# Performance work log

Hardware: AMD Instinct MI355X
Metric: run time of the kernel (lower is better)

## Reference

```python
import jax, jax.numpy as jnp
import numpy as np

M_TOP = 30      # top-M candidates per query
K_NB = 20       # K+1 nearest within candidate set (K=19)
BETA = 0.15


def setup_inputs() -> dict:
    key = jax.random.key(0)
    k1, k2, k3 = jax.random.split(key, 3)
    N, D, B, R = 500000, 512, 4096, 1000
    X = jax.random.normal(k1, (N, D), dtype=jnp.float32)
    Q = jax.random.normal(k2, (B, D), dtype=jnp.float32)
    ranks = jax.random.randint(k3, (R, B), 0, N, dtype=jnp.int64)
    return {"X": X, "Q": Q, "ranks": ranks}


def reference(X, Q, ranks):
    # ranks: [n_ranked, B] -> take top-M candidate ids per query: [B, M]
    rt = ranks.T[:, :M_TOP]                       # [B, M]
    Xt = X[rt]                                    # gather: [B, M, D]
    # batched self-similarity among the M candidates
    sim = jnp.einsum('bmd,bnd->bmn', Xt, Xt)      # [B, M, M]
    # descending sort, keep top K_NB values+indices (== -sort(-sim)[:K], argsort(-sim)[:K])
    vals, idx = jax.lax.top_k(sim, K_NB)          # [B, M, K]
    # weights: first neighbor (self) weight 1.0, rest scaled by beta
    w = jnp.concatenate([jnp.ones_like(vals[..., :1]), vals[..., 1:] * BETA], axis=-1)
    w = w[..., None]                              # [B, M, K, 1]
    # gather neighbor descriptors within each query's candidate set
    # x_g[b,m,k,d] = Xt[b, idx[b,m,k], d]
    x_g = jnp.take_along_axis(Xt[:, None, :, :], idx[..., None], axis=2)  # [B, M, K, D]
    # weighted average over the K neighbors
    x_dba = jnp.sum(x_g * w, axis=2) / jnp.sum(w, axis=2)                 # [B, M, D]
    # rerank candidates against the query descriptor
    scores = jnp.einsum('bd,bmd->bm', Q, x_dba)   # [B, M]
    order = jnp.argsort(-scores, axis=-1)         # [B, M]
    rerank = jnp.take_along_axis(rt, order, axis=1)  # [B, M] final db ids
    return rerank, scores, order, x_dba
```

## Files before the change

### kernel.cpp

```cpp
#include <hip/hip_runtime.h>
#include <stdint.h>

#define MT   30
#define KNB  20
#define DD   512
#define SROW 68
#define WSTRIDE 960

#define PR(r) ((((r) & 1) * 15) + ((r) >> 1))

extern "C" __global__ void __launch_bounds__(256, 8)
mdesc_decide(const float* __restrict__ X, const float* __restrict__ Q,
             const int* __restrict__ ranks, float* __restrict__ out,
             float* __restrict__ wsF, int B)
{
    __shared__ alignas(16) char arrA[MT * SROW * 4];
    __shared__ alignas(16) float QS[DD];
    __shared__ double simS[MT][MT + 1];
    __shared__ double qdotPart[MT][8];
    __shared__ double qdotS[MT];
    __shared__ int    rtS[MT];

    float  (*XtS)[SROW] = (float(*)[SROW])arrA;
    float  (*MwS)[MT]   = (float(*)[MT])arrA;
    double *scoreS      = (double*)(arrA + 3600);
    int    *orderS      = (int*)(arrA + 3840);

    const int b = blockIdx.x;
    const int tid = threadIdx.x;

    if (tid < MT) rtS[tid] = ranks[(size_t)tid * B + b];
    __syncthreads();

    const bool isSim = (tid < 120);
    const bool isQ   = (tid >= 128 && tid < 248);
    int i0 = 0, i1 = 0, j0 = 0, j1 = 0;
    if (isSim) {
        int I = 0, rem = tid;
        while (rem >= 15 - I) { rem -= 15 - I; ++I; }
        int J = I + rem;
        i0 = 2 * I; i1 = i0 + 1; j0 = 2 * J; j1 = j0 + 1;
    }
    const int qm = (tid - 128) >> 2;
    const int qs = (tid - 128) & 3;

    double a00 = 0.0, a01 = 0.0, a10 = 0.0, a11 = 0.0;

    for (int st = 0; st < 8; ++st) {
        for (int i = tid; i < MT * 16; i += 256) {
            int row = i >> 4;
            int k = i & 15;
            float4 v = *(const float4*)(X + (size_t)rtS[row] * DD + st * 64 + (k << 2));
            *(float4*)(&XtS[PR(row)][k << 2]) = v;
        }
        if (st == 0 && tid < 128) {
            float4 v = *(const float4*)(Q + (size_t)b * DD + (tid << 2));
            *(float4*)(&QS[tid << 2]) = v;
        }
        __syncthreads();

        if (isSim) {
            const float* R0 = &XtS[PR(i0)][0];
            const float* R1 = &XtS[PR(i1)][0];
            const float* C0 = &XtS[PR(j0)][0];
            const float* C1 = &XtS[PR(j1)][0];
            for (int k = 0; k < 16; ++k) {
                float4 va0 = *(const float4*)(R0 + (k << 2));
                float4 va1 = *(const float4*)(R1 + (k << 2));
                float4 vb0 = *(const float4*)(C0 + (k << 2));
                float4 vb1 = *(const float4*)(C1 + (k << 2));
                const float* A0 = (const float*)&va0;
                const float* A1 = (const float*)&va1;
                const float* B0 = (const float*)&vb0;
                const float* B1 = (const float*)&vb1;
                #pragma unroll
                for (int c = 0; c < 4; ++c) {
                    double x0 = (double)A0[c], x1 = (double)A1[c];
                    double y0 = (double)B0[c], y1 = (double)B1[c];
                    a00 = fma(x0, y0, a00);
                    a01 = fma(x0, y1, a01);
                    a10 = fma(x1, y0, a10);
                    a11 = fma(x1, y1, a11);
                }
            }
            if (st == 3) {
                simS[i0][j0] = a00; simS[i0][j1] = a01;
                simS[i1][j0] = a10; simS[i1][j1] = a11;
                a00 = a01 = a10 = a11 = 0.0;
            }
            if (st == 7) {
                double s00 = simS[i0][j0] + a00;
                double s01 = simS[i0][j1] + a01;
                double s10 = simS[i1][j0] + a10;
                double s11 = simS[i1][j1] + a11;
                simS[i0][j0] = s00; simS[j0][i0] = s00;
                simS[i0][j1] = s01; simS[j1][i0] = s01;
                simS[i1][j0] = s10; simS[j0][i1] = s10;
                simS[i1][j1] = s11; simS[j1][i1] = s11;
            }
        }
        if (isQ && (st & 3) == qs) {
            double acc = 0.0;
            const float* xr = &XtS[PR(qm)][0];
            for (int k = 0; k < 16; ++k) {
                float4 q4 = *(const float4*)(&QS[(st * 16 + k) << 2]);
                float4 x4 = *(const float4*)(xr + (k << 2));
                const float* qq = (const float*)&q4;
                const float* xx = (const float*)&x4;
                #pragma unroll
                for (int c = 0; c < 4; ++c)
                    acc = fma((double)qq[c], (double)xx[c], acc);
            }
            qdotPart[qm][st] = acc;
        }
        __syncthreads();
    }

    for (int i = tid; i < MT * MT; i += 256) (&MwS[0][0])[i] = 0.0f;
    __syncthreads();

    const size_t sec = (size_t)B * MT;
    if (tid < MT) {
        {
            double acc = 0.0;
            #pragma unroll
            for (int s = 0; s < 8; ++s) acc += qdotPart[tid][s];
            qdotS[tid] = acc;
        }
        const int m = tid;
        unsigned used = 0;
        double Wsum = 0.0, sAcc = 0.0;
        for (int k = 0; k < KNB; ++k) {
            double best = -1.0e300; int bj = 0;
            for (int j = 0; j < MT; ++j) {
                if (used & (1u << j)) continue;
                double v = simS[m][j];
                if (v > best) { best = v; bj = j; }
            }
            used |= (1u << bj);
            double w = (k == 0) ? 1.0 : best * 0.15;
            Wsum += w;
            sAcc = fma(w, qdotS[bj], sAcc);
            MwS[m][bj] = (float)w;
        }
        scoreS[m] = sAcc / Wsum;
        float inv = (float)(1.0 / Wsum);
        for (int j = 0; j < MT; ++j)
            if (used & (1u << j)) MwS[m][j] *= inv;
        double mysc = scoreS[tid];
        int pos = 0;
        for (int j = 0; j < MT; ++j) {
            double v = scoreS[j];
            if (v > mysc || (v == mysc && j < tid)) ++pos;
        }
        orderS[pos] = tid;
        int r = tid;
        int src = orderS[r];
        out[(size_t)b * MT + r]            = (float)rtS[src];
        out[sec + (size_t)b * MT + tid]    = (float)scoreS[tid];
        out[2 * sec + (size_t)b * MT + r]  = (float)src;
    }
    __syncthreads();

    for (int i = tid; i < MT * MT; i += 256)
        wsF[(size_t)b * WSTRIDE + i] = (&MwS[0][0])[i];
}

extern "C" __global__ void __launch_bounds__(256)
mdesc_xdba(const float* __restrict__ X, const int* __restrict__ ranks,
           const float* __restrict__ wsF, float* __restrict__ out, int B)
{
    __shared__ float wS[MT][MT];
    __shared__ int   rtS[MT];

    const int b = blockIdx.x;
    const int tid = threadIdx.x;

    if (tid < MT) rtS[tid] = ranks[(size_t)tid * B + b];
    for (int i = tid; i < MT * MT; i += 256)
        (&wS[0][0])[i] = wsF[(size_t)b * WSTRIDE + i];
    __syncthreads();

    const int c  = tid & 127;
    const int g  = tid >> 7;
    const int r0 = g * 15;

    float4 acc[15];
    #pragma unroll
    for (int r = 0; r < 15; ++r) acc[r] = make_float4(0.f, 0.f, 0.f, 0.f);

    for (int j = 0; j < MT; ++j) {
        float4 xv = *(const float4*)(X + (size_t)rtS[j] * DD + (c << 2));
        #pragma unroll
        for (int r = 0; r < 15; ++r) {
            float wj = wS[r0 + r][j];
            acc[r].x = fmaf(wj, xv.x, acc[r].x);
            acc[r].y = fmaf(wj, xv.y, acc[r].y);
            acc[r].z = fmaf(wj, xv.z, acc[r].z);
            acc[r].w = fmaf(wj, xv.w, acc[r].w);
        }
    }

    const size_t xbase = 3 * (size_t)B * MT;
    #pragma unroll
    for (int r = 0; r < 15; ++r) {
        *(float4*)(out + xbase + ((size_t)b * MT + (r0 + r)) * DD + (c << 2)) = acc[r];
    }
}

extern "C" void kernel_launch(void* const* d_in, const int* in_sizes, int n_in,
                              void* d_out, int out_size, void* d_ws, size_t ws_size,
                              hipStream_t stream)
{
    const float* X = (const float*)d_in[0];
    const float* Q = (const float*)d_in[1];
    const int* ranks = (const int*)d_in[2];
    const int B = in_sizes[1] / DD;
    float* wsF = (float*)d_ws;
    mdesc_decide<<<dim3(B), dim3(256), 0, stream>>>(X, Q, ranks, (float*)d_out, wsF, B);
    mdesc_xdba<<<dim3(B), dim3(256), 0, stream>>>(X, ranks, wsF, (float*)d_out, B);
}
```

Measured before the change: 275.0 us.

## Fuse neighbor-selection and weighted-average kernels into one launch

Merges the decision kernel and the x_dba accumulation kernel into a single kernel, keeping the weight matrix in shared memory (padded to 32 columns) instead of writing it to a workspace and reloading it. This removes one kernel launch and a global round trip of the weights. The inner loop now processes two candidate rows per iteration with float2 weight loads. Launch bounds drop from 8 to 6 waves per SIMD, which allows more registers but may lower occupancy. Fusing also serialises the latency-bound gather phase behind the selection phase within each block.

Result: faster. 248.6 us, median of 2 (-9.6%).

```diff
diff --git a/kernel.cpp b/kernel.cpp
--- a/kernel.cpp
+++ b/kernel.cpp
@@ -5,14 +5,13 @@
 #define KNB  20
 #define DD   512
 #define SROW 68
-#define WSTRIDE 960
+#define MWS  32
 
 #define PR(r) ((((r) & 1) * 15) + ((r) >> 1))
 
-extern "C" __global__ void __launch_bounds__(256, 8)
-mdesc_decide(const float* __restrict__ X, const float* __restrict__ Q,
-             const int* __restrict__ ranks, float* __restrict__ out,
-             float* __restrict__ wsF, int B)
+extern "C" __global__ void __launch_bounds__(256, 6)
+mdesc_fused(const float* __restrict__ X, const float* __restrict__ Q,
+            const int* __restrict__ ranks, float* __restrict__ out, int B)
 {
     __shared__ alignas(16) char arrA[MT * SROW * 4];
     __shared__ alignas(16) float QS[DD];
@@ -22,9 +21,9 @@
     __shared__ int    rtS[MT];
 
     float  (*XtS)[SROW] = (float(*)[SROW])arrA;
-    float  (*MwS)[MT]   = (float(*)[MT])arrA;
-    double *scoreS      = (double*)(arrA + 3600);
-    int    *orderS      = (int*)(arrA + 3840);
+    float  (*MwS)[MWS]  = (float(*)[MWS])arrA;
+    double *scoreS      = (double*)(arrA + 3840);
+    int    *orderS      = (int*)(arrA + 4080);
 
     const int b = blockIdx.x;
     const int tid = threadIdx.x;
@@ -116,7 +115,7 @@
         __syncthreads();
     }
 
-    for (int i = tid; i < MT * MT; i += 256) (&MwS[0][0])[i] = 0.0f;
+    for (int i = tid; i < MT * MWS; i += 256) (&MwS[0][0])[i] = 0.0f;
     __syncthreads();
 
     const size_t sec = (size_t)B * MT;
@@ -162,49 +161,37 @@
     }
     __syncthreads();
 
-    for (int i = tid; i < MT * MT; i += 256)
-        wsF[(size_t)b * WSTRIDE + i] = (&MwS[0][0])[i];
-}
-
-extern "C" __global__ void __launch_bounds__(256)
-mdesc_xdba(const float* __restrict__ X, const int* __restrict__ ranks,
-           const float* __restrict__ wsF, float* __restrict__ out, int B)
-{
-    __shared__ float wS[MT][MT];
-    __shared__ int   rtS[MT];
-
-    const int b = blockIdx.x;
-    const int tid = threadIdx.x;
-
-    if (tid < MT) rtS[tid] = ranks[(size_t)tid * B + b];
-    for (int i = tid; i < MT * MT; i += 256)
-        (&wS[0][0])[i] = wsF[(size_t)b * WSTRIDE + i];
-    __syncthreads();
-
-    const int c  = tid & 127;
-    const int g  = tid >> 7;
-    const int r0 = g * 15;
-
-    float4 acc[15];
-    #pragma unroll
-    for (int r = 0; r < 15; ++r) acc[r] = make_float4(0.f, 0.f, 0.f, 0.f);
-
-    for (int j = 0; j < MT; ++j) {
-        float4 xv = *(const float4*)(X + (size_t)rtS[j] * DD + (c << 2));
+    {
+        const int sub = tid >> 7;
+        const int c   = tid & 127;
+        const int r0  = sub * 15;
+        float4 acc[15];
+        #pragma unroll
+        for (int r = 0; r < 15; ++r) acc[r] = make_float4(0.f, 0.f, 0.f, 0.f);
+
+        for (int jg = 0; jg < 15; ++jg) {
+            const int ja = 2 * jg, jb = ja + 1;
+            float4 xv0 = *(const float4*)(X + (size_t)rtS[ja] * DD + (c << 2));
+            float4 xv1 = *(const float4*)(X + (size_t)rtS[jb] * DD + (c << 2));
+            #pragma unroll
+            for (int r = 0; r < 15; ++r) {
+                float2 wv = *(const float2*)&MwS[r0 + r][ja];
+                acc[r].x = fmaf(wv.x, xv0.x, acc[r].x);
+                acc[r].x = fmaf(wv.y, xv1.x, acc[r].x);
+                acc[r].y = fmaf(wv.x, xv0.y, acc[r].y);
+                acc[r].y = fmaf(wv.y, xv1.y, acc[r].y);
+                acc[r].z = fmaf(wv.x, xv0.z, acc[r].z);
+                acc[r].z = fmaf(wv.y, xv1.z, acc[r].z);
+                acc[r].w = fmaf(wv.x, xv0.w, acc[r].w);
+                acc[r].w = fmaf(wv.y, xv1.w, acc[r].w);
+            }
+        }
+
+        const size_t xbase = 3 * sec;
         #pragma unroll
         for (int r = 0; r < 15; ++r) {
-            float wj = wS[r0 + r][j];
-            acc[r].x = fmaf(wj, xv.x, acc[r].x);
-            acc[r].y = fmaf(wj, xv.y, acc[r].y);
-            acc[r].z = fmaf(wj, xv.z, acc[r].z);
-            acc[r].w = fmaf(wj, xv.w, acc[r].w);
-        }
-    }
-
-    const size_t xbase = 3 * (size_t)B * MT;
-    #pragma unroll
-    for (int r = 0; r < 15; ++r) {
-        *(float4*)(out + xbase + ((size_t)b * MT + (r0 + r)) * DD + (c << 2)) = acc[r];
+            *(float4*)(out + xbase + ((size_t)b * MT + (r0 + r)) * DD + (c << 2)) = acc[r];
+        }
     }
 }
 
@@ -216,7 +203,5 @@
     const float* Q = (const float*)d_in[1];
     const int* ranks = (const int*)d_in[2];
     const int B = in_sizes[1] / DD;
-    float* wsF = (float*)d_ws;
-    mdesc_decide<<<dim3(B), dim3(256), 0, stream>>>(X, Q, ranks, (float*)d_out, wsF, B);
-    mdesc_xdba<<<dim3(B), dim3(256), 0, stream>>>(X, ranks, wsF, (float*)d_out, B);
+    mdesc_fused<<<dim3(B), dim3(256), 0, stream>>>(X, Q, ranks, (float*)d_out, B);
 }
```
